# Kernel optimization log

Hardware: AMD Instinct MI355X
Metric: run time of the kernel (lower is better)

Reference implementation:

```python
import jax, jax.numpy as jnp
import numpy as np

N_DOCS = 500_000
VOCAB = 30522
NNZ_PER_DOC = 64
NNZ = N_DOCS * NNZ_PER_DOC
Q_NNZ = 64
TOP_K = 10


def setup_inputs() -> dict:
    key = jax.random.key(0)
    k1, k2, k3, k4 = jax.random.split(key, 4)
    # sparse query in COO form: [1, q_nnz] indices into vocab, [1, q_nnz] values
    indices = jax.random.randint(k1, (1, Q_NNZ), 0, VOCAB, dtype=jnp.int32)
    values = jax.random.normal(k2, (1, Q_NNZ), dtype=jnp.float32)
    # CSR collection matrix [N_DOCS, VOCAB], fixed nnz per row for generation
    crow = jnp.arange(N_DOCS + 1, dtype=jnp.int32) * NNZ_PER_DOC
    col = jax.random.randint(k3, (NNZ,), 0, VOCAB, dtype=jnp.int32)
    vals = jax.random.normal(k4, (NNZ,), dtype=jnp.float32) * 0.1
    return {"indices": indices, "values": values, "crow": crow, "col": col, "vals": vals}


def reference(indices, values, crow, col, vals):
    # densify sparse COO query (duplicates sum, matching to_dense of uncoalesced COO)
    query = jnp.zeros((VOCAB,), jnp.float32).at[indices[0]].add(values[0])
    # CSR SpMV: per-nnz contribution = vals * query[col], segment-sum by row
    nnz = vals.shape[0]
    row_ids = jnp.searchsorted(crow, jnp.arange(nnz, dtype=crow.dtype), side="right") - 1
    contrib = vals * query[col]
    scores = jax.ops.segment_sum(contrib, row_ids, num_segments=N_DOCS)  # [N_DOCS]
    top_vals, top_idx = jax.lax.top_k(scores, TOP_K)
    return top_vals, top_idx
```

## Files before the change

kernel.cpp:

```cpp
#include <hip/hip_runtime.h>
#include <math.h>

constexpr int       VOCAB    = 30522;
constexpr int       N_DOCS   = 500000;
constexpr long long NNZ      = (long long)N_DOCS * 64;
constexpr int       Q_NNZ    = 64;
constexpr int       TOP_K    = 10;
constexpr int       BM_WORDS = (VOCAB + 31) / 32;

constexpr int STREAM_BLOCKS = 2048;
constexpr int TOPK_BLOCKS   = 128;

typedef int int4v __attribute__((ext_vector_type(4)));

__device__ __forceinline__ void topk_insert(float (&tv)[TOP_K], int (&ti)[TOP_K],
                                            float v, int vi) {
    if (v > tv[TOP_K - 1] || (v == tv[TOP_K - 1] && vi < ti[TOP_K - 1])) {
#pragma unroll
        for (int k = 0; k < TOP_K; ++k) {
            bool better = (v > tv[k]) || (v == tv[k] && vi < ti[k]);
            if (better) { float a = tv[k]; int b = ti[k]; tv[k] = v; ti[k] = vi; v = a; vi = b; }
        }
    }
}

template <int S0>
__device__ void merge_tree(float* sv, int* si, int t) {
    for (int s = S0; s >= 1; s >>= 1) {
        if (t < s) {
            const int a = t * TOP_K, b = (t + s) * TOP_K;
            float mv[TOP_K]; int mi[TOP_K];
            int i = 0, j = 0;
#pragma unroll
            for (int k = 0; k < TOP_K; ++k) {
                float av = sv[a + i], bv = sv[b + j];
                int   ai = si[a + i], bi = si[b + j];
                bool ta = (av > bv) || (av == bv && ai <= bi);
                mv[k] = ta ? av : bv;
                mi[k] = ta ? ai : bi;
                if (ta) ++i; else ++j;
            }
#pragma unroll
            for (int k = 0; k < TOP_K; ++k) { sv[a + k] = mv[k]; si[a + k] = mi[k]; }
        }
        __syncthreads();
    }
}

__global__ __launch_bounds__(256) void zero_scores(float4* __restrict__ s) {
    const int i = blockIdx.x * 256 + threadIdx.x;
    if (i < N_DOCS / 4) s[i] = float4{0.0f, 0.0f, 0.0f, 0.0f};
}

__global__ void build_query(const int* __restrict__ qidx,
                            const float* __restrict__ qval,
                            float* __restrict__ qdense) {
    __shared__ int   sidx[Q_NNZ];
    __shared__ float sval[Q_NNZ];
    const int i = threadIdx.x;
    sidx[i] = qidx[i];
    sval[i] = qval[i];
    __syncthreads();
    const int qi = sidx[i];
    float s = 0.0f;
    for (int j = 0; j < Q_NNZ; ++j)
        if (sidx[j] == qi) s += sval[j];
    qdense[qi] = s;
}

__global__ __launch_bounds__(256) void spmv_stream(const int* __restrict__ qidx,
                                                   const float* __restrict__ qdense,
                                                   const int* __restrict__ col,
                                                   const float* __restrict__ vals,
                                                   float* __restrict__ scores) {
    __shared__ unsigned bm[BM_WORDS];
    for (int i = threadIdx.x; i < BM_WORDS; i += 256) bm[i] = 0u;
    __syncthreads();
    if (threadIdx.x < Q_NNZ) {
        int c = qidx[threadIdx.x];
        atomicOr(&bm[c >> 5], 1u << (c & 31));
    }
    __syncthreads();

    const long long nvec   = NNZ / 4;
    const long long stride = (long long)STREAM_BLOCKS * 256;

#pragma unroll 4
    for (long long v = (long long)blockIdx.x * 256 + threadIdx.x; v < nvec; v += stride) {
        const int4v c4 = *(const int4v*)(col + v * 4);

        const unsigned h0 = (bm[(unsigned)c4.x >> 5] >> (c4.x & 31)) & 1u;
        const unsigned h1 = (bm[(unsigned)c4.y >> 5] >> (c4.y & 31)) & 1u;
        const unsigned h2 = (bm[(unsigned)c4.z >> 5] >> (c4.z & 31)) & 1u;
        const unsigned h3 = (bm[(unsigned)c4.w >> 5] >> (c4.w & 31)) & 1u;

        if (h0 | h1 | h2 | h3) {
            float s = 0.0f;
            if (h0) s += vals[v * 4 + 0] * qdense[c4.x];
            if (h1) s += vals[v * 4 + 1] * qdense[c4.y];
            if (h2) s += vals[v * 4 + 2] * qdense[c4.z];
            if (h3) s += vals[v * 4 + 3] * qdense[c4.w];
            atomicAdd(&scores[(int)(v >> 4)], s);
        }
    }
}

__global__ __launch_bounds__(256) void topk_partial(const float* __restrict__ scores,
                                                    float* __restrict__ cand_v,
                                                    int* __restrict__ cand_i) {
    float tv[TOP_K]; int ti[TOP_K];
#pragma unroll
    for (int k = 0; k < TOP_K; ++k) { tv[k] = -INFINITY; ti[k] = 0x7fffffff; }

    const int tid    = blockIdx.x * blockDim.x + threadIdx.x;
    const int stride = gridDim.x * blockDim.x;
    for (int i = tid; i < N_DOCS; i += stride) {
        const float v = scores[i];
        if (v > tv[TOP_K - 1]) topk_insert(tv, ti, v, i);
    }

    __shared__ float sv[256 * TOP_K];
    __shared__ int   si[256 * TOP_K];
    const int t = threadIdx.x;
#pragma unroll
    for (int k = 0; k < TOP_K; ++k) { sv[t * TOP_K + k] = tv[k]; si[t * TOP_K + k] = ti[k]; }
    __syncthreads();

    merge_tree<128>(sv, si, t);

    if (t == 0) {
        for (int k = 0; k < TOP_K; ++k) {
            cand_v[blockIdx.x * TOP_K + k] = sv[k];
            cand_i[blockIdx.x * TOP_K + k] = si[k];
        }
    }
}

__global__ __launch_bounds__(256) void topk_final(const float* __restrict__ cand_v,
                                                  const int* __restrict__ cand_i,
                                                  float* __restrict__ out) {
    __shared__ float sv[256 * TOP_K];
    __shared__ int   si[256 * TOP_K];
    const int t = threadIdx.x;

    if (t < TOPK_BLOCKS) {
        for (int k = 0; k < TOP_K; ++k) {
            sv[t * TOP_K + k] = cand_v[t * TOP_K + k];
            si[t * TOP_K + k] = cand_i[t * TOP_K + k];
        }
    } else {
        for (int k = 0; k < TOP_K; ++k) {
            sv[t * TOP_K + k] = -INFINITY;
            si[t * TOP_K + k] = 0x7fffffff;
        }
    }
    __syncthreads();

    merge_tree<128>(sv, si, t);

    if (t == 0) {
        for (int k = 0; k < TOP_K; ++k) {
            out[k]         = sv[k];
            out[TOP_K + k] = (float)si[k];
        }
    }
}

extern "C" void kernel_launch(void* const* d_in, const int* in_sizes, int n_in,
                              void* d_out, int out_size, void* d_ws, size_t ws_size,
                              hipStream_t stream) {
    const int*   qidx = (const int*)  d_in[0];
    const float* qval = (const float*)d_in[1];
    const int*   col  = (const int*)  d_in[3];
    const float* vals = (const float*)d_in[4];
    float* out = (float*)d_out;

    char* ws = (char*)d_ws;
    float* scores = (float*)ws;
    size_t off = (size_t)N_DOCS * 4;
    float* qdense = (float*)(ws + off);
    off += (size_t)((VOCAB * 4 + 127) & ~127);
    float* cand_v = (float*)(ws + off);
    off += (size_t)TOPK_BLOCKS * TOP_K * 4;
    int* cand_i = (int*)(ws + off);

    zero_scores<<<(N_DOCS / 4 + 255) / 256, 256, 0, stream>>>((float4*)scores);
    build_query<<<1, Q_NNZ, 0, stream>>>(qidx, qval, qdense);
    spmv_stream<<<STREAM_BLOCKS, 256, 0, stream>>>(qidx, qdense, col, vals, scores);
    topk_partial<<<TOPK_BLOCKS, 256, 0, stream>>>(scores, cand_v, cand_i);
    topk_final<<<1, 256, 0, stream>>>(cand_v, cand_i, out);
}
```

Baseline: 73.04 us.

## Batch col loads per thread and compact hits into shared queue for dense gather

The SpMV stream loop is fully unrolled into two batches of eight independent 16-byte col loads per thread, so more memory requests are in flight before the bitmap tests run. Hits are no longer processed in place inside divergent branches. They are packed into a shared-memory work queue and processed by all threads after a barrier. This compacts the sparse vals/qdense gathers and the score atomics onto fully active lanes. The cost is extra shared memory and a block-wide barrier, re-reading col for each queued hit, and a fallback path if the queue overflows.

```diff
diff --git a/kernel.cpp b/kernel.cpp
--- a/kernel.cpp
+++ b/kernel.cpp
@@ -8,8 +8,12 @@
 constexpr int       TOP_K    = 10;
 constexpr int       BM_WORDS = (VOCAB + 31) / 32;
 
-constexpr int STREAM_BLOCKS = 2048;
-constexpr int TOPK_BLOCKS   = 128;
+constexpr int NV4          = (int)(NNZ / 4);
+constexpr int SPMV_BLOCKS  = 2048;
+constexpr int GSTRIDE      = SPMV_BLOCKS * 256;
+constexpr int NU           = (NV4 + GSTRIDE - 1) / GSTRIDE;
+constexpr int QCAP         = 1024;
+constexpr int TOPK_BLOCKS  = 128;
 
 typedef int int4v __attribute__((ext_vector_type(4)));
 
@@ -74,34 +78,77 @@
                                                    const float* __restrict__ vals,
                                                    float* __restrict__ scores) {
     __shared__ unsigned bm[BM_WORDS];
-    for (int i = threadIdx.x; i < BM_WORDS; i += 256) bm[i] = 0u;
-    __syncthreads();
-    if (threadIdx.x < Q_NNZ) {
-        int c = qidx[threadIdx.x];
+    __shared__ unsigned queue[QCAP];
+    __shared__ int qcount;
+
+    const int t = threadIdx.x;
+    for (int i = t; i < BM_WORDS; i += 256) bm[i] = 0u;
+    if (t == 0) qcount = 0;
+    __syncthreads();
+    if (t < Q_NNZ) {
+        int c = qidx[t];
         atomicOr(&bm[c >> 5], 1u << (c & 31));
     }
     __syncthreads();
 
-    const long long nvec   = NNZ / 4;
-    const long long stride = (long long)STREAM_BLOCKS * 256;
-
-#pragma unroll 4
-    for (long long v = (long long)blockIdx.x * 256 + threadIdx.x; v < nvec; v += stride) {
-        const int4v c4 = *(const int4v*)(col + v * 4);
-
-        const unsigned h0 = (bm[(unsigned)c4.x >> 5] >> (c4.x & 31)) & 1u;
-        const unsigned h1 = (bm[(unsigned)c4.y >> 5] >> (c4.y & 31)) & 1u;
-        const unsigned h2 = (bm[(unsigned)c4.z >> 5] >> (c4.z & 31)) & 1u;
-        const unsigned h3 = (bm[(unsigned)c4.w >> 5] >> (c4.w & 31)) & 1u;
-
-        if (h0 | h1 | h2 | h3) {
-            float s = 0.0f;
-            if (h0) s += vals[v * 4 + 0] * qdense[c4.x];
-            if (h1) s += vals[v * 4 + 1] * qdense[c4.y];
-            if (h2) s += vals[v * 4 + 2] * qdense[c4.z];
-            if (h3) s += vals[v * 4 + 3] * qdense[c4.w];
-            atomicAdd(&scores[(int)(v >> 4)], s);
-        }
+    const int tid0 = blockIdx.x * 256 + t;
+
+#pragma unroll
+    for (int half = 0; half < 2; ++half) {
+        int4v    d[8];
+        unsigned vld[8];
+
+#pragma unroll
+        for (int j = 0; j < 8; ++j) {
+            const int u = half * 8 + j;
+            int v = tid0 + u * GSTRIDE;
+            vld[j] = (v < NV4) ? 1u : 0u;
+            v = vld[j] ? v : 0;
+            d[j] = *(const int4v*)(col + (size_t)v * 4);
+        }
+
+#pragma unroll
+        for (int j = 0; j < 8; ++j) {
+            const int u = half * 8 + j;
+            unsigned m = 0;
+            m |= ((bm[(unsigned)d[j].x >> 5] >> (d[j].x & 31)) & 1u) << 0;
+            m |= ((bm[(unsigned)d[j].y >> 5] >> (d[j].y & 31)) & 1u) << 1;
+            m |= ((bm[(unsigned)d[j].z >> 5] >> (d[j].z & 31)) & 1u) << 2;
+            m |= ((bm[(unsigned)d[j].w >> 5] >> (d[j].w & 31)) & 1u) << 3;
+            m *= vld[j];
+            if (m) {
+                const unsigned rec = ((unsigned)t << 8) | ((unsigned)u << 4) | m;
+                const int slot = atomicAdd(&qcount, 1);
+                if (slot < QCAP) {
+                    queue[slot] = rec;
+                } else {
+                    const int v = tid0 + u * GSTRIDE;
+                    float s = 0.0f;
+                    if (m & 1u) s += vals[(size_t)v * 4 + 0] * qdense[d[j].x];
+                    if (m & 2u) s += vals[(size_t)v * 4 + 1] * qdense[d[j].y];
+                    if (m & 4u) s += vals[(size_t)v * 4 + 2] * qdense[d[j].z];
+                    if (m & 8u) s += vals[(size_t)v * 4 + 3] * qdense[d[j].w];
+                    atomicAdd(&scores[v >> 4], s);
+                }
+            }
+        }
+    }
+    __syncthreads();
+
+    const int n = min(qcount, QCAP);
+    for (int e = t; e < n; e += 256) {
+        const unsigned rec = queue[e];
+        const int      rt  = (int)((rec >> 8) & 255u);
+        const int      u   = (int)((rec >> 4) & 15u);
+        const unsigned m   = rec & 15u;
+        const int      v   = blockIdx.x * 256 + rt + u * GSTRIDE;
+        const int4v c4 = *(const int4v*)(col + (size_t)v * 4);
+        float s = 0.0f;
+        if (m & 1u) s += vals[(size_t)v * 4 + 0] * qdense[c4.x];
+        if (m & 2u) s += vals[(size_t)v * 4 + 1] * qdense[c4.y];
+        if (m & 4u) s += vals[(size_t)v * 4 + 2] * qdense[c4.z];
+        if (m & 8u) s += vals[(size_t)v * 4 + 3] * qdense[c4.w];
+        atomicAdd(&scores[v >> 4], s);
     }
 }
 
@@ -186,7 +233,7 @@
 
     zero_scores<<<(N_DOCS / 4 + 255) / 256, 256, 0, stream>>>((float4*)scores);
     build_query<<<1, Q_NNZ, 0, stream>>>(qidx, qval, qdense);
-    spmv_stream<<<STREAM_BLOCKS, 256, 0, stream>>>(qidx, qdense, col, vals, scores);
+    spmv_stream<<<SPMV_BLOCKS, 256, 0, stream>>>(qidx, qdense, col, vals, scores);
     topk_partial<<<TOPK_BLOCKS, 256, 0, stream>>>(scores, cand_v, cand_i);
     topk_final<<<1, 256, 0, stream>>>(cand_v, cand_i, out);
 }
```

After: 74.54 us. +2.1%, slower.

## Stream column indices via direct global-to-LDS loads with double-buffered chunks per wave

Applied to the files above, without the earlier changes.

Each wave now owns eight contiguous 512-int chunks of the column array and streams them into LDS through global_load_lds with double buffering and explicit vmcnt waits. It records a per-lane hit bitmask during the scan and only goes back to global memory for vals, col and qdense on hits. The goal is to keep more bytes in flight and cut VGPR pressure in the bandwidth-bound col scan. It adds LDS traffic, re-reads col on hits, and assumes the grid exactly covers NNZ (2048*4*8*512 = 33.5M >= 32M).

```diff
diff --git a/kernel.cpp b/kernel.cpp
--- a/kernel.cpp
+++ b/kernel.cpp
@@ -8,10 +8,20 @@
 constexpr int       TOP_K    = 10;
 constexpr int       BM_WORDS = (VOCAB + 31) / 32;
 
-constexpr int STREAM_BLOCKS = 2048;
-constexpr int TOPK_BLOCKS   = 128;
+constexpr int CHUNK_INTS   = 512;
+constexpr int NCHUNK       = (int)(NNZ / CHUNK_INTS);
+constexpr int SPMV_BLOCKS  = 2048;
+constexpr int WAVES_TOTAL  = SPMV_BLOCKS * 4;
+constexpr int CHUNKS_PER_W = 8;
+constexpr int TOPK_BLOCKS  = 128;
 
 typedef int int4v __attribute__((ext_vector_type(4)));
+typedef __attribute__((address_space(1))) const void* gas_cptr;
+typedef __attribute__((address_space(3))) void*       las_ptr;
+
+__device__ __forceinline__ void glds16(const int* g, int* lds_base) {
+    __builtin_amdgcn_global_load_lds((gas_cptr)g, (las_ptr)lds_base, 16, 0, 0);
+}
 
 __device__ __forceinline__ void topk_insert(float (&tv)[TOP_K], int (&ti)[TOP_K],
                                             float v, int vi) {
@@ -74,33 +84,83 @@
                                                    const float* __restrict__ vals,
                                                    float* __restrict__ scores) {
     __shared__ unsigned bm[BM_WORDS];
-    for (int i = threadIdx.x; i < BM_WORDS; i += 256) bm[i] = 0u;
-    __syncthreads();
-    if (threadIdx.x < Q_NNZ) {
-        int c = qidx[threadIdx.x];
+    __shared__ int stage[4][2][CHUNK_INTS];
+
+    const int t = threadIdx.x;
+    for (int i = t; i < BM_WORDS; i += 256) bm[i] = 0u;
+    __syncthreads();
+    if (t < Q_NNZ) {
+        int c = qidx[t];
         atomicOr(&bm[c >> 5], 1u << (c & 31));
     }
     __syncthreads();
 
-    const long long nvec   = NNZ / 4;
-    const long long stride = (long long)STREAM_BLOCKS * 256;
-
-#pragma unroll 4
-    for (long long v = (long long)blockIdx.x * 256 + threadIdx.x; v < nvec; v += stride) {
-        const int4v c4 = *(const int4v*)(col + v * 4);
-
-        const unsigned h0 = (bm[(unsigned)c4.x >> 5] >> (c4.x & 31)) & 1u;
-        const unsigned h1 = (bm[(unsigned)c4.y >> 5] >> (c4.y & 31)) & 1u;
-        const unsigned h2 = (bm[(unsigned)c4.z >> 5] >> (c4.z & 31)) & 1u;
-        const unsigned h3 = (bm[(unsigned)c4.w >> 5] >> (c4.w & 31)) & 1u;
-
-        if (h0 | h1 | h2 | h3) {
-            float s = 0.0f;
-            if (h0) s += vals[v * 4 + 0] * qdense[c4.x];
-            if (h1) s += vals[v * 4 + 1] * qdense[c4.y];
-            if (h2) s += vals[v * 4 + 2] * qdense[c4.z];
-            if (h3) s += vals[v * 4 + 3] * qdense[c4.w];
-            atomicAdd(&scores[(int)(v >> 4)], s);
+    const int lane = t & 63;
+    const int w    = t >> 6;
+    const int cb0  = (blockIdx.x * 4 + w) * CHUNKS_PER_W;
+
+    int* const buf0 = &stage[w][0][0];
+    int* const buf1 = &stage[w][1][0];
+
+#define ISSUE(CIDX, BUF) { \
+        const int cc_ = min((CIDX), NCHUNK - 1); \
+        const int* src_ = col + (size_t)cc_ * CHUNK_INTS + lane * 4; \
+        int* dst_ = (BUF) ? buf1 : buf0; \
+        glds16(src_,       dst_);         \
+        glds16(src_ + 256, dst_ + 256);   \
+    }
+
+    ISSUE(cb0, 0)
+
+    unsigned long long hitmask = 0;
+
+#pragma unroll
+    for (int it = 0; it < CHUNKS_PER_W; ++it) {
+        if (it < CHUNKS_PER_W - 1) {
+            ISSUE(cb0 + it + 1, (it + 1) & 1)
+            asm volatile("s_waitcnt vmcnt(2)" ::: "memory");
+        } else {
+            asm volatile("s_waitcnt vmcnt(0)" ::: "memory");
+        }
+        __builtin_amdgcn_sched_barrier(0);
+
+        const int* b = (it & 1) ? buf1 : buf0;
+        const int4v a0 = *(const int4v*)(b + lane * 4);
+        const int4v a1 = *(const int4v*)(b + 256 + lane * 4);
+
+        unsigned m = 0;
+        m |= ((bm[(unsigned)a0.x >> 5] >> (a0.x & 31)) & 1u) << 0;
+        m |= ((bm[(unsigned)a0.y >> 5] >> (a0.y & 31)) & 1u) << 1;
+        m |= ((bm[(unsigned)a0.z >> 5] >> (a0.z & 31)) & 1u) << 2;
+        m |= ((bm[(unsigned)a0.w >> 5] >> (a0.w & 31)) & 1u) << 3;
+        m |= ((bm[(unsigned)a1.x >> 5] >> (a1.x & 31)) & 1u) << 4;
+        m |= ((bm[(unsigned)a1.y >> 5] >> (a1.y & 31)) & 1u) << 5;
+        m |= ((bm[(unsigned)a1.z >> 5] >> (a1.z & 31)) & 1u) << 6;
+        m |= ((bm[(unsigned)a1.w >> 5] >> (a1.w & 31)) & 1u) << 7;
+        if (cb0 + it >= NCHUNK) m = 0;
+
+        hitmask |= (unsigned long long)m << (it * 8);
+    }
+#undef ISSUE
+
+    if (hitmask) {
+#pragma unroll
+        for (int c = 0; c < CHUNKS_PER_W; ++c) {
+            const unsigned mb = (unsigned)(hitmask >> (c * 8)) & 255u;
+            if (!mb) continue;
+            const int gc = cb0 + c;
+#pragma unroll
+            for (int s = 0; s < 2; ++s) {
+                const unsigned nib = (mb >> (s * 4)) & 15u;
+                if (!nib) continue;
+                const size_t base = (size_t)gc * CHUNK_INTS + s * 256 + lane * 4;
+                float acc = 0.0f;
+                if (nib & 1u) acc += vals[base + 0] * qdense[col[base + 0]];
+                if (nib & 2u) acc += vals[base + 1] * qdense[col[base + 1]];
+                if (nib & 4u) acc += vals[base + 2] * qdense[col[base + 2]];
+                if (nib & 8u) acc += vals[base + 3] * qdense[col[base + 3]];
+                atomicAdd(&scores[base >> 6], acc);
+            }
         }
     }
 }
@@ -186,7 +246,7 @@
 
     zero_scores<<<(N_DOCS / 4 + 255) / 256, 256, 0, stream>>>((float4*)scores);
     build_query<<<1, Q_NNZ, 0, stream>>>(qidx, qval, qdense);
-    spmv_stream<<<STREAM_BLOCKS, 256, 0, stream>>>(qidx, qdense, col, vals, scores);
+    spmv_stream<<<SPMV_BLOCKS, 256, 0, stream>>>(qidx, qdense, col, vals, scores);
     topk_partial<<<TOPK_BLOCKS, 256, 0, stream>>>(scores, cand_v, cand_i);
     topk_final<<<1, 256, 0, stream>>>(cand_v, cand_i, out);
 }
```

New measurement: 79.98 us. +9.5%, slower.
